# Performance work log

Hardware: AMD Instinct MI355X
Metric: run time of the kernel (lower is better)

The kernel has to match this reference:

```python
import jax, jax.numpy as jnp
import numpy as np
from functools import partial

# --- constants from module init / yolov5 NMS conventions ---
CONF_THRES = 0.25
IOU_THRES = 0.45
PATCH_CONF = 0.001
GN = jnp.array([640.0, 640.0, 640.0, 640.0])  # img_size[[1,0,1,0]]
MAX_WH = 4096.0       # per-class NMS offset trick
K_CLEAN = 256         # fixed-size cap for clean detections (max_det=1000 effectively)
K_PATCH = 1024        # fixed-size cap for patch detections (max_det=30000 effectively)
MAXDET_CLEAN = 1000
MAXDET_PATCH = 30000
B, N, NC = 8, 25200, 80


def xywh2xyxy(x):
    xy, wh = x[..., :2], x[..., 2:4]
    return jnp.concatenate([xy - wh * 0.5, xy + wh * 0.5], axis=-1)


def pairwise_iou(a, b):
    # a: [A,4], b: [B,4] -> [A,B] jaccard overlap (same math as IoU.get_iou)
    tl = jnp.maximum(a[:, None, :2], b[None, :, :2])
    br = jnp.minimum(a[:, None, 2:], b[None, :, 2:])
    wh = jnp.clip(br - tl, 0.0)
    inter = wh[..., 0] * wh[..., 1]
    area_a = (a[:, 2] - a[:, 0]) * (a[:, 3] - a[:, 1])
    area_b = (b[:, 2] - b[:, 0]) * (b[:, 3] - b[:, 1])
    return inter / (area_a[:, None] + area_b[None, :] - inter)


def greedy_nms(iou_mat, valid, iou_thres):
    # iou_mat: [K,K] (score-sorted order), valid: [K] bool. Greedy suppression.
    K = valid.shape[0]
    j = jnp.arange(K)

    def body(i, keep):
        suppress = keep[i] & (iou_mat[i] > iou_thres) & (j > i)
        return keep & ~suppress

    return jax.lax.fori_loop(0, K, body, valid)


def _nms_single(pred, conf_thres, K, max_det):
    # pred: [N, 5+nc] raw yolov5 prediction for one image
    boxes = xywh2xyxy(pred[:, :4])
    obj = pred[:, 4]
    cls_scores = pred[:, 5:] * obj[:, None]          # conf = obj * cls
    conf = cls_scores.max(axis=-1)
    cls = jnp.argmax(cls_scores, axis=-1).astype(pred.dtype)
    valid = (obj > conf_thres) & (conf > conf_thres)
    mscore = jnp.where(valid, conf, -1.0)
    _, idx = jax.lax.top_k(mscore, K)                # fixed-size candidate prefilter
    bk, ck, vk = boxes[idx], cls[idx], valid[idx]
    off_boxes = bk + (ck * MAX_WH)[:, None]          # class-offset NMS
    iou = pairwise_iou(off_boxes, off_boxes)
    keep = greedy_nms(jax.lax.stop_gradient(iou), vk, IOU_THRES)
    keep = keep & (jnp.cumsum(keep.astype(jnp.int32)) <= max_det)
    return bk, ck, keep


def _forward(output_clean, output_patch):
    nms_clean = jax.vmap(lambda p: _nms_single(p, CONF_THRES, K_CLEAN, MAXDET_CLEAN))
    nms_patch = jax.vmap(lambda p: _nms_single(p, PATCH_CONF, K_PATCH, MAXDET_PATCH))
    bc, cc, kc = nms_clean(output_clean)   # [B,Kc,4],[B,Kc],[B,Kc]
    bp, cp, kp = nms_patch(output_patch)   # [B,Kp,4],[B,Kp],[B,Kp]
    bc_n = bc / GN
    bp_n = bp / GN

    def per_img(bp_i, cp_i, kp_i, bc_i, cc_i, kc_i):
        iou = pairwise_iou(bp_i, bc_i)                       # [Kp, Kc]
        match = kp_i[:, None] & (cp_i[:, None] == cc_i[None, :])
        tm = jnp.max(jnp.where(match, iou, 0.0), axis=0)     # max IoU per clean det
        return jnp.sum(jnp.where(kc_i, tm, 0.0)), jnp.sum(kc_i.astype(jnp.float32))

    sums, counts = jax.vmap(per_img)(bp_n, cp, kp, bc_n, cc, kc)
    total, cnt = sums.sum(), counts.sum()
    return jnp.where(cnt > 0, 1.0 - total / jnp.maximum(cnt, 1.0), 1.0)


def setup_inputs() -> dict:
    key = jax.random.key(0)
    k1, k2 = jax.random.split(key)

    def make(k):
        kxy, kwh, ko, kc = jax.random.split(k, 4)
        xy = jax.random.uniform(kxy, (B, N, 2)) * 608.0 + 16.0   # centers in-frame
        wh = jax.random.uniform(kwh, (B, N, 2)) * 96.0 + 8.0     # plausible box sizes
        obj = jax.random.uniform(ko, (B, N, 1))
        cls = jax.random.uniform(kc, (B, N, NC))
        return jnp.concatenate([xy, wh, obj, cls], axis=-1)

    return {"output_clean": make(k1), "output_patch": make(k2)}


def reference(output_clean, output_patch):
    return _forward(output_clean, output_patch)
```

## Files before the change

### kernel.cpp

```cpp
#include <hip/hip_runtime.h>

#define N_ANCH 25200
#define NCLS   80
#define ROW    85
#define NIMG   16
#define KMAX   1024
#define NBINS  1024
#define CAND_CAP 4096
#define SC2_RPC 16
#define SC2_CPI 1575
#define SC2_CFLOATS (SC2_RPC*ROW)
#define SC2_BPI 96
#define SC2_WPI 192
#define PCHUNK 64
#define CCNT_STRIDE 16

typedef unsigned long long u64;
typedef unsigned int u32;

#define OFF_KEYS 0ull
#define OFF_HIST 3225600ull
#define OFF_TBIN 3291136ull
#define OFF_CCNT 3291200ull
#define OFF_CAND 3292224ull
#define OFF_SEL  3816512ull
#define OFF_BOX  3947584ull
#define OFF_CLS  4209728ull
#define OFF_RINIT 4275264ull
#define OFF_KEEP 4277312ull
#define WS_NEED  4342848ull
#define ZERO_BYTES 66624ull

#define DMA16(gsrc, ldst) \
    __builtin_amdgcn_global_load_lds( \
        (const __attribute__((address_space(1))) void*)(gsrc), \
        (__attribute__((address_space(3))) void*)(ldst), 16, 0, 0)

__device__ __forceinline__ int key_bin(u64 key) {
    u32 hi = (u32)(key >> 32);
    if (hi == 0u) return 0;
    float conf = __uint_as_float(hi - 0x40000000u);
    int b = 1 + (int)(conf * 1022.0f);
    return b > 1023 ? 1023 : b;
}

__device__ __forceinline__ u64 readlane64(u64 v, int src) {
    u32 lo = (u32)__builtin_amdgcn_readlane((int)(u32)(v & 0xffffffffull), src);
    u32 hi = (u32)__builtin_amdgcn_readlane((int)(u32)(v >> 32), src);
    return ((u64)hi << 32) | (u64)lo;
}

__device__ __forceinline__ u64 shfl64_xor(u64 v, int m) {
    int lo = __shfl_xor((int)(u32)(v & 0xffffffffull), m, 64);
    int hi = __shfl_xor((int)(u32)(v >> 32), m, 64);
    return ((u64)(u32)hi << 32) | (u64)(u32)lo;
}

__device__ __forceinline__ void sc_issue(const float* __restrict__ img, int ch,
                                         int lane, float* buf)
{
    const float* s = img + (size_t)ch * SC2_CFLOATS;
    #pragma unroll
    for (int u = 0; u < 5; ++u)
        DMA16(s + u * 256 + lane * 4, buf + u * 256);
    if (lane < 20)
        DMA16(s + 1280 + lane * 4, buf + 1280);
}

__device__ __forceinline__ void sc_compute(int b, int c, int lane, const float* buf,
                                           u64* __restrict__ keys, int* bh)
{
    const int r = lane & 15, h = lane >> 4;
    const float* p = buf + r * ROW;
    const float obj = p[4];
    float best = -1.0f; int bc = 0;
    #pragma unroll
    for (int d = 0; d < 20; ++d) {
        const float s = p[5 + h * 20 + d] * obj;
        if (s > best) { best = s; bc = h * 20 + d; }
    }
    #pragma unroll
    for (int m = 16; m <= 32; m <<= 1) {
        const float o = __shfl_xor(best, m, 64);
        const int  oc = __shfl_xor(bc, m, 64);
        if (o > best || (o == best && oc < bc)) { best = o; bc = oc; }
    }
    if (h == 0) {
        const int n = c * SC2_RPC + r;
        const float th = (b < 8) ? 0.25f : 0.001f;
        const bool valid = (obj > th) && (best > th);
        const u32 hi = valid ? (__float_as_uint(best) + 0x40000000u) : 0u;
        if (valid) {
            int bin = 1 + (int)(best * 1022.0f);
            if (bin > 1023) bin = 1023;
            atomicAdd(&bh[bin], 1);
        }
        const u32 nbar = 32767u - (u32)n;
        keys[(size_t)b * N_ANCH + n] =
            ((u64)hi << 32) | ((u64)nbar << 8) | (u64)(u32)bc;
    }
}

__global__ __launch_bounds__(128) void k_score(const float* __restrict__ clean,
                                               const float* __restrict__ patch,
                                               u64* __restrict__ keys,
                                               int* __restrict__ hist)
{
    __shared__ float lds[2][2][SC2_CFLOATS];
    __shared__ int bh[NBINS];
    const int t = threadIdx.x;
    const int wv = t >> 6, lane = t & 63;
    const int b = blockIdx.x / SC2_BPI;
    const int blk = blockIdx.x - b * SC2_BPI;
    const int wimg = blk * 2 + wv;
    for (int i = t; i < NBINS; i += 128) bh[i] = 0;
    __syncthreads();
    const float* img = (b < 8) ? clean + (size_t)b * N_ANCH * ROW
                               : patch + (size_t)(b - 8) * N_ANCH * ROW;
    int cur = 0;
    sc_issue(img, wimg, lane, &lds[wv][0][0]);
    for (int c = wimg; c < SC2_CPI; c += SC2_WPI) {
        const int cn = c + SC2_WPI;
        if (cn < SC2_CPI) {
            sc_issue(img, cn, lane, &lds[wv][cur ^ 1][0]);
            asm volatile("s_waitcnt vmcnt(6)" ::: "memory");
        } else {
            asm volatile("s_waitcnt vmcnt(0)" ::: "memory");
        }
        __builtin_amdgcn_sched_barrier(0);
        sc_compute(b, c, lane, &lds[wv][cur][0], keys, bh);
        cur ^= 1;
    }
    __syncthreads();
    for (int i = t; i < NBINS; i += 128)
        if (bh[i]) atomicAdd(&hist[b * NBINS + i], bh[i]);
}

__global__ __launch_bounds__(256) void k_thresh(const int* __restrict__ hist,
                                                int* __restrict__ tbin)
{
    __shared__ int arr[256];
    const int b = blockIdx.x;
    const int t = threadIdx.x;
    int hh[4];
    hh[0] = hist[b * NBINS + 4 * t + 0];
    hh[1] = hist[b * NBINS + 4 * t + 1];
    hh[2] = hist[b * NBINS + 4 * t + 2];
    hh[3] = hist[b * NBINS + 4 * t + 3];
    const int r = hh[0] + hh[1] + hh[2] + hh[3];
    arr[t] = r;
    __syncthreads();
    for (int off = 1; off < 256; off <<= 1) {
        int v = (t + off < 256) ? arr[t + off] : 0;
        __syncthreads();
        arr[t] += v;
        __syncthreads();
    }
    const int K = (b < 8) ? 256 : 1024;
    int cb = arr[t] - r;
    for (int d = 3; d >= 0; --d) {
        int ca = cb + hh[d];
        if (cb < K && ca >= K) tbin[b] = 4 * t + d;
        cb = ca;
    }
}

__global__ __launch_bounds__(256) void k_compact(const u64* __restrict__ keys,
                                                 const int* __restrict__ tbin,
                                                 int* __restrict__ ccnt,
                                                 u64* __restrict__ cand)
{
    const int b = blockIdx.x;
    const int T = tbin[b];
    const u64* kp = keys + (size_t)b * N_ANCH;
    const int start = blockIdx.y * 1575;
    const int lane = threadIdx.x & 63;
    #pragma unroll
    for (int it = 0; it < 7; ++it) {
        const int off = it * 256 + threadIdx.x;
        const bool in = off < 1575;
        const u64 key = in ? kp[start + off] : 0ull;
        const bool cnd = in && (key_bin(key) >= T);
        const u64 bal = __ballot(cnd);
        if (bal) {
            int base = 0;
            if (lane == 0) base = atomicAdd(&ccnt[b * CCNT_STRIDE], __popcll(bal));
            base = __shfl(base, 0, 64);
            if (cnd) {
                const int pos = base + __popcll(bal & ((1ull << lane) - 1ull));
                if (pos < CAND_CAP) cand[(size_t)b * CAND_CAP + pos] = key;
            }
        }
    }
}

__global__ __launch_bounds__(1024) void k_sort(const u64* __restrict__ cand,
                                               const int* __restrict__ ccnt,
                                               u64* __restrict__ sel)
{
    __shared__ u64 sk[CAND_CAP];
    const int b = blockIdx.x;
    const int C = min(ccnt[b * CCNT_STRIDE], CAND_CAP);
    const int t = threadIdx.x;
    u64 e0, e1, e2, e3;
    e0 = (t < C) ? cand[(size_t)b * CAND_CAP + t] : 0ull;
    e1 = (1024 + t < C) ? cand[(size_t)b * CAND_CAP + 1024 + t] : 0ull;
    e2 = (2048 + t < C) ? cand[(size_t)b * CAND_CAP + 2048 + t] : 0ull;
    e3 = (3072 + t < C) ? cand[(size_t)b * CAND_CAP + 3072 + t] : 0ull;
    #define CSWAP_D(a, c) { if ((a) < (c)) { u64 _t = (a); (a) = (c); (c) = _t; } }
    #define CSWAP_A(a, c) { if ((a) > (c)) { u64 _t = (a); (a) = (c); (c) = _t; } }
    for (int k = 2; k <= 4096; k <<= 1) {
        for (int j = k >> 1; j > 0; j >>= 1) {
            if (j >= 1024) {
                if (j == 2048) { CSWAP_D(e0, e2); CSWAP_D(e1, e3); }
                else {
                    if (k == 4096) { CSWAP_D(e0, e1); CSWAP_D(e2, e3); }
                    else           { CSWAP_D(e0, e1); CSWAP_A(e2, e3); }
                }
            } else if (j >= 64) {
                __syncthreads();
                sk[t] = e0; sk[1024 + t] = e1; sk[2048 + t] = e2; sk[3072 + t] = e3;
                __syncthreads();
                const int tp = t ^ j;
                #pragma unroll
                for (int p = 0; p < 4; ++p) {
                    const int i = p * 1024 + t;
                    const u64 cv = (p == 0) ? e0 : (p == 1) ? e1 : (p == 2) ? e2 : e3;
                    const u64 o = sk[p * 1024 + tp];
                    const bool take_max = (((i & k) == 0) == ((t & j) == 0));
                    const u64 mx = cv > o ? cv : o;
                    const u64 mn = cv > o ? o : cv;
                    const u64 nv = take_max ? mx : mn;
                    if (p == 0) e0 = nv; else if (p == 1) e1 = nv;
                    else if (p == 2) e2 = nv; else e3 = nv;
                }
            } else {
                #pragma unroll
                for (int p = 0; p < 4; ++p) {
                    const int i = p * 1024 + t;
                    const u64 cv = (p == 0) ? e0 : (p == 1) ? e1 : (p == 2) ? e2 : e3;
                    const u64 o = shfl64_xor(cv, j);
                    const bool take_max = (((i & k) == 0) == ((t & j) == 0));
                    const u64 mx = cv > o ? cv : o;
                    const u64 mn = cv > o ? o : cv;
                    const u64 nv = take_max ? mx : mn;
                    if (p == 0) e0 = nv; else if (p == 1) e1 = nv;
                    else if (p == 2) e2 = nv; else e3 = nv;
                }
            }
        }
    }
    const int K = (b < 8) ? 256 : 1024;
    if (t < K) sel[b * KMAX + t] = e0;
    #undef CSWAP_D
    #undef CSWAP_A
}

__global__ __launch_bounds__(1024) void k_nms_mask(const float* __restrict__ clean,
                                                   const float* __restrict__ patch,
                                                   const u64* __restrict__ sel,
                                                   float4* __restrict__ boxes,
                                                   int* __restrict__ cls,
                                                   u64* __restrict__ rinit,
                                                   u64* __restrict__ mask,
                                                   u64* __restrict__ diag)
{
    __shared__ float4 bx[KMAX];
    __shared__ float ar[KMAX];
    const int b = blockIdx.x, y = blockIdx.y;
    const int K = (b < 8) ? 256 : 1024;
    const int row0 = y * 64;
    if (row0 >= K) return;
    const int t = threadIdx.x;
    {
        const u64 key = (t < K) ? sel[b * KMAX + t] : 0ull;
        const u32 hi = (u32)(key >> 32);
        const bool valid = (t < K) && (hi != 0u);
        const u64 bal = __ballot(valid);
        if (y == 0 && (t & 63) == 0) rinit[b * 16 + (t >> 6)] = ~bal;
        if (t < K) {
            const int n = 32767 - (int)((key >> 8) & 0x7FFFu);
            const int c = (int)(key & 0x7Fu);
            const float* src = ((b < 8) ? (clean + (size_t)b * N_ANCH * ROW)
                                        : (patch + (size_t)(b - 8) * N_ANCH * ROW))
                               + (size_t)n * ROW;
            const float x = src[0], yy = src[1], w = src[2], h = src[3];
            const float4 raw = make_float4(x - w * 0.5f, yy - h * 0.5f,
                                           x + w * 0.5f, yy + h * 0.5f);
            if (y == 0) { boxes[b * KMAX + t] = raw; cls[b * KMAX + t] = c; }
            const float off = (float)c * 4096.0f;
            const float4 ob = make_float4(raw.x + off, raw.y + off,
                                          raw.z + off, raw.w + off);
            bx[t] = ob;
            ar[t] = (ob.z - ob.x) * (ob.w - ob.y);
        }
    }
    __syncthreads();
    const int w   = t >> 6;
    const int row = row0 + (t & 63);
    u64* dst = mask + ((size_t)b * KMAX + row) * 16 + w;
    if (((w << 6) + 63) <= row0 && row0 > 0) { *dst = 0ull; return; }
    const float4 bi = bx[row];
    const float ai = ar[row];
    const int jbase = w << 6;
    u64 m = 0;
    #pragma unroll 8
    for (int k = 0; k < 64; ++k) {
        const int j = jbase + k;
        const float4 bj = bx[j];
        const float ax = fmaxf(bi.x, bj.x), ay = fmaxf(bi.y, bj.y);
        const float bx2 = fminf(bi.z, bj.z), by2 = fminf(bi.w, bj.w);
        const float iw = fmaxf(bx2 - ax, 0.f), ih = fmaxf(by2 - ay, 0.f);
        const float inter = iw * ih;
        const float iou = inter / (ai + ar[j] - inter);
        if (j > row && iou > 0.45f) m |= (1ull << k);
    }
    *dst = m;
    if (w == (row0 >> 6)) diag[(size_t)b * KMAX + row] = m;
}

__global__ __launch_bounds__(1024) void k_nms_scan(const u64* __restrict__ mask,
                                                   const u64* __restrict__ diag,
                                                   const u64* __restrict__ rinit,
                                                   int* __restrict__ keep)
{
    extern __shared__ u64 smem[];
    const int b = blockIdx.x;
    const int K = (b < 8) ? 256 : 1024;
    const int W = K >> 6;
    const int t = threadIdx.x;
    u64* smask = smem;
    u64* sdiag = smem + (size_t)K * 16;
    {
        const float4* s4 = (const float4*)(mask + (size_t)b * KMAX * 16);
        float4* d4 = (float4*)smask;
        const int n4 = (K * 16) >> 1;
        for (int i = t; i < n4; i += 1024) d4[i] = s4[i];
        const float4* s4d = (const float4*)(diag + (size_t)b * KMAX);
        float4* d4d = (float4*)sdiag;
        for (int i = t; i < (K >> 1); i += 1024) d4d[i] = s4d[i];
    }
    __syncthreads();
    if (t >= 64) return;
    const int lane = t;
    const int q = lane >> 4;
    const int wl = lane & 15;
    u64 w_remv = rinit[b * 16 + wl];
    u64 ow = readlane64(w_remv, 0);
    u64 dj = sdiag[lane];
    for (int g = 0; g < W; ++g) {
        u64 nz = __ballot(dj != 0ull);
        u64 o = ow;
        while (nz) {
            const int j = (int)__builtin_ctzll(nz);
            nz &= nz - 1;
            if (!((o >> j) & 1ull)) o |= readlane64(dj, j);
        }
        const u64 kept = ~o;
        if (g + 1 < W) dj = sdiag[(g + 1) * 64 + lane];
        const u64* mrow = smask + (size_t)(g * 64 + q * 16) * 16 + wl;
        const u32 kg = (u32)((kept >> (q * 16)) & 0xFFFFull);
        u64 a0 = 0, a1 = 0;
        #pragma unroll
        for (int i = 0; i < 16; i += 2) {
            const u64 m0 = mrow[(size_t)(i + 0) * 16];
            const u64 m1 = mrow[(size_t)(i + 1) * 16];
            a0 |= ((kg >> i) & 1u) ? m0 : 0ull;
            a1 |= ((kg >> (i + 1)) & 1u) ? m1 : 0ull;
        }
        u64 part = a0 | a1;
        part |= shfl64_xor(part, 16);
        part |= shfl64_xor(part, 32);
        w_remv |= part;
        if (g + 1 < W) ow = readlane64(w_remv, g + 1);
    }
    if (lane < W) {
        #pragma unroll
        for (int k = 0; k < 64; ++k)
            keep[b * KMAX + lane * 64 + k] = (int)(((w_remv >> k) & 1) ^ 1ull);
    }
}

__global__ __launch_bounds__(256) void k_match_partial(const float4* __restrict__ boxes,
                                                       const int* __restrict__ cls,
                                                       const int* __restrict__ keep,
                                                       float* __restrict__ pmax)
{
    __shared__ float4 pb[PCHUNK];
    __shared__ float par[PCHUNK];
    __shared__ int pcls[PCHUNK];
    const int c = blockIdx.x;
    const int p = blockIdx.y;
    const int bp = 8 + c;
    const int t = threadIdx.x;
    if (t < PCHUNK) {
        const int i = p * PCHUNK + t;
        const float4 v = boxes[bp * KMAX + i];
        pb[t] = v;
        par[t] = (v.z - v.x) * (v.w - v.y);
        pcls[t] = keep[bp * KMAX + i] ? cls[bp * KMAX + i] : -1;
    }
    __syncthreads();
    const float4 bc = boxes[c * KMAX + t];
    const int cc = cls[c * KMAX + t];
    const float area_c = (bc.z - bc.x) * (bc.w - bc.y);
    float tm = 0.f;
    #pragma unroll 8
    for (int i = 0; i < PCHUNK; ++i) {
        const float4 bi = pb[i];
        const float ax = fmaxf(bi.x, bc.x), ay = fmaxf(bi.y, bc.y);
        const float bx2 = fminf(bi.z, bc.z), by2 = fminf(bi.w, bc.w);
        const float iw = fmaxf(bx2 - ax, 0.f), ih = fmaxf(by2 - ay, 0.f);
        const float inter = iw * ih;
        const float iou = inter / (par[i] + area_c - inter);
        tm = fmaxf(tm, (pcls[i] == cc) ? iou : 0.f);
    }
    pmax[(c * 16 + p) * 256 + t] = tm;
}

__global__ __launch_bounds__(256) void k_match_final(const float* __restrict__ pmax,
                                                     const int* __restrict__ keep,
                                                     float* __restrict__ out)
{
    __shared__ float red[8];
    const int t = threadIdx.x;
    float tot = 0.f, cn = 0.f;
    for (int c = 0; c < 8; ++c) {
        float tm = 0.f;
        #pragma unroll
        for (int p = 0; p < 16; ++p)
            tm = fmaxf(tm, pmax[(c * 16 + p) * 256 + t]);
        const int kc = keep[c * KMAX + t];
        float val = kc ? tm : 0.f;
        float cv  = kc ? 1.f : 0.f;
        for (int off = 32; off > 0; off >>= 1) {
            val += __shfl_down(val, off);
            cv  += __shfl_down(cv, off);
        }
        const int wv = t >> 6, lane = t & 63;
        if (lane == 0) { red[wv] = val; red[4 + wv] = cv; }
        __syncthreads();
        if (t == 0) {
            tot += red[0] + red[1] + red[2] + red[3];
            cn  += red[4] + red[5] + red[6] + red[7];
        }
        __syncthreads();
    }
    if (t == 0)
        out[0] = (cn > 0.f) ? (1.0f - tot / fmaxf(cn, 1.0f)) : 1.0f;
}

extern "C" void kernel_launch(void* const* d_in, const int* in_sizes, int n_in,
                              void* d_out, int out_size, void* d_ws, size_t ws_size,
                              hipStream_t stream)
{
    if (ws_size < WS_NEED) return;
    const float* clean = (const float*)d_in[0];
    const float* patch = (const float*)d_in[1];
    float* out = (float*)d_out;
    char* ws = (char*)d_ws;

    u64*    keys = (u64*)(ws + OFF_KEYS);
    u64*    mask = (u64*)(ws + OFF_KEYS);
    int*    hist = (int*)(ws + OFF_HIST);
    int*    tbin = (int*)(ws + OFF_TBIN);
    int*    ccnt = (int*)(ws + OFF_CCNT);
    u64*    cand = (u64*)(ws + OFF_CAND);
    u64*    diag = (u64*)(ws + OFF_CAND);
    float*  pmax = (float*)(ws + OFF_CAND);
    u64*    sel  = (u64*)(ws + OFF_SEL);
    float4* boxes = (float4*)(ws + OFF_BOX);
    int*    cls  = (int*)(ws + OFF_CLS);
    u64*    rinit = (u64*)(ws + OFF_RINIT);
    int*    keep = (int*)(ws + OFF_KEEP);

    hipMemsetAsync(ws + OFF_HIST, 0, ZERO_BYTES, stream);

    k_score<<<NIMG * SC2_BPI, 128, 0, stream>>>(clean, patch, keys, hist);
    k_thresh<<<NIMG, 256, 0, stream>>>(hist, tbin);
    k_compact<<<dim3(NIMG, 16), 256, 0, stream>>>(keys, tbin, ccnt, cand);
    k_sort<<<NIMG, 1024, 0, stream>>>(cand, ccnt, sel);
    k_nms_mask<<<dim3(NIMG, 16), 1024, 0, stream>>>(clean, patch, sel, boxes, cls,
                                                    rinit, mask, diag);
    k_nms_scan<<<NIMG, 1024, KMAX * 16 * 8 + KMAX * 8, stream>>>(mask, diag, rinit, keep);
    k_match_partial<<<dim3(8, 16), 256, 0, stream>>>(boxes, cls, keep, pmax);
    k_match_final<<<1, 256, 0, stream>>>(pmax, keep, out);
}
```

Baseline: 133.6 us.

## Fuse threshold, compaction and sort into one kernel; register-staged score loads

Merges the histogram-threshold, candidate compaction and bitonic sort kernels into a single per-image kernel. Candidates now go straight into shared memory, which removes two launches and the global candidate round trip. The scoring kernel swaps its async global-to-LDS DMA double buffering for register double buffering followed by an LDS store, and raises the block count per image. The trade-off is that compaction now runs on only 16 blocks, one per image, scanning 25200 keys each, so that phase has far less parallelism.

Measured after the change: 174.4 us. +30.5%, slower.

```diff
diff --git a/kernel.cpp b/kernel.cpp
--- a/kernel.cpp
+++ b/kernel.cpp
@@ -10,31 +10,23 @@
 #define SC2_RPC 16
 #define SC2_CPI 1575
 #define SC2_CFLOATS (SC2_RPC*ROW)
-#define SC2_BPI 96
-#define SC2_WPI 192
+#define SC3_BPI 160
+#define SC3_WPI 320
 #define PCHUNK 64
-#define CCNT_STRIDE 16
 
 typedef unsigned long long u64;
 typedef unsigned int u32;
 
 #define OFF_KEYS 0ull
 #define OFF_HIST 3225600ull
-#define OFF_TBIN 3291136ull
-#define OFF_CCNT 3291200ull
-#define OFF_CAND 3292224ull
-#define OFF_SEL  3816512ull
-#define OFF_BOX  3947584ull
-#define OFF_CLS  4209728ull
-#define OFF_RINIT 4275264ull
-#define OFF_KEEP 4277312ull
-#define WS_NEED  4342848ull
-#define ZERO_BYTES 66624ull
-
-#define DMA16(gsrc, ldst) \
-    __builtin_amdgcn_global_load_lds( \
-        (const __attribute__((address_space(1))) void*)(gsrc), \
-        (__attribute__((address_space(3))) void*)(ldst), 16, 0, 0)
+#define OFF_DIAG 3291136ull
+#define OFF_SEL  3422208ull
+#define OFF_BOX  3553280ull
+#define OFF_CLS  3815424ull
+#define OFF_RINIT 3880960ull
+#define OFF_KEEP 3883008ull
+#define WS_NEED  3948544ull
+#define ZERO_BYTES 65536ull
 
 __device__ __forceinline__ int key_bin(u64 key) {
     u32 hi = (u32)(key >> 32);
@@ -56,15 +48,27 @@
     return ((u64)(u32)hi << 32) | (u64)(u32)lo;
 }
 
-__device__ __forceinline__ void sc_issue(const float* __restrict__ img, int ch,
-                                         int lane, float* buf)
-{
-    const float* s = img + (size_t)ch * SC2_CFLOATS;
-    #pragma unroll
-    for (int u = 0; u < 5; ++u)
-        DMA16(s + u * 256 + lane * 4, buf + u * 256);
-    if (lane < 20)
-        DMA16(s + 1280 + lane * 4, buf + 1280);
+__device__ __forceinline__ void ld6(const float* __restrict__ img, int ch, int lane,
+                                    float4* f)
+{
+    const float4* s = (const float4*)(img + (size_t)ch * SC2_CFLOATS);
+    f[0] = s[lane];
+    f[1] = s[lane + 64];
+    f[2] = s[lane + 128];
+    f[3] = s[lane + 192];
+    f[4] = s[lane + 256];
+    if (lane < 20) f[5] = s[lane + 320];
+}
+
+__device__ __forceinline__ void st6(float* buf, int lane, const float4* f)
+{
+    float4* d = (float4*)buf;
+    d[lane]       = f[0];
+    d[lane + 64]  = f[1];
+    d[lane + 128] = f[2];
+    d[lane + 192] = f[3];
+    d[lane + 256] = f[4];
+    if (lane < 20) d[lane + 320] = f[5];
 }
 
 __device__ __forceinline__ void sc_compute(int b, int c, int lane, const float* buf,
@@ -106,107 +110,89 @@
                                                u64* __restrict__ keys,
                                                int* __restrict__ hist)
 {
-    __shared__ float lds[2][2][SC2_CFLOATS];
+    __shared__ float lds[2][SC2_CFLOATS];
     __shared__ int bh[NBINS];
     const int t = threadIdx.x;
     const int wv = t >> 6, lane = t & 63;
-    const int b = blockIdx.x / SC2_BPI;
-    const int blk = blockIdx.x - b * SC2_BPI;
+    const int b = blockIdx.x / SC3_BPI;
+    const int blk = blockIdx.x - b * SC3_BPI;
     const int wimg = blk * 2 + wv;
     for (int i = t; i < NBINS; i += 128) bh[i] = 0;
     __syncthreads();
     const float* img = (b < 8) ? clean + (size_t)b * N_ANCH * ROW
                                : patch + (size_t)(b - 8) * N_ANCH * ROW;
-    int cur = 0;
-    sc_issue(img, wimg, lane, &lds[wv][0][0]);
-    for (int c = wimg; c < SC2_CPI; c += SC2_WPI) {
-        const int cn = c + SC2_WPI;
-        if (cn < SC2_CPI) {
-            sc_issue(img, cn, lane, &lds[wv][cur ^ 1][0]);
-            asm volatile("s_waitcnt vmcnt(6)" ::: "memory");
+    float* buf = &lds[wv][0];
+    float4 fA[6], fB[6];
+    bool useA = true;
+    if (wimg < SC2_CPI) ld6(img, wimg, lane, fA);
+    for (int c = wimg; c < SC2_CPI; c += SC3_WPI) {
+        const int cn = c + SC3_WPI;
+        if (useA) {
+            if (cn < SC2_CPI) ld6(img, cn, lane, fB);
+            st6(buf, lane, fA);
         } else {
-            asm volatile("s_waitcnt vmcnt(0)" ::: "memory");
-        }
-        __builtin_amdgcn_sched_barrier(0);
-        sc_compute(b, c, lane, &lds[wv][cur][0], keys, bh);
-        cur ^= 1;
+            if (cn < SC2_CPI) ld6(img, cn, lane, fA);
+            st6(buf, lane, fB);
+        }
+        sc_compute(b, c, lane, buf, keys, bh);
+        useA = !useA;
     }
     __syncthreads();
     for (int i = t; i < NBINS; i += 128)
         if (bh[i]) atomicAdd(&hist[b * NBINS + i], bh[i]);
 }
 
-__global__ __launch_bounds__(256) void k_thresh(const int* __restrict__ hist,
-                                                int* __restrict__ tbin)
-{
-    __shared__ int arr[256];
+__global__ __launch_bounds__(1024) void k_tcs(const u64* __restrict__ keys,
+                                              const int* __restrict__ hist,
+                                              u64* __restrict__ sel)
+{
+    __shared__ u64 sk[CAND_CAP];
+    __shared__ int arr[NBINS];
+    __shared__ int cnt;
+    __shared__ int Tsh;
     const int b = blockIdx.x;
     const int t = threadIdx.x;
-    int hh[4];
-    hh[0] = hist[b * NBINS + 4 * t + 0];
-    hh[1] = hist[b * NBINS + 4 * t + 1];
-    hh[2] = hist[b * NBINS + 4 * t + 2];
-    hh[3] = hist[b * NBINS + 4 * t + 3];
-    const int r = hh[0] + hh[1] + hh[2] + hh[3];
-    arr[t] = r;
-    __syncthreads();
-    for (int off = 1; off < 256; off <<= 1) {
-        int v = (t + off < 256) ? arr[t + off] : 0;
+    const int K = (b < 8) ? 256 : 1024;
+    if (t == 0) { cnt = 0; Tsh = 0; }
+    const int h = hist[b * NBINS + t];
+    arr[t] = h;
+    __syncthreads();
+    for (int off = 1; off < NBINS; off <<= 1) {
+        int v = (t + off < NBINS) ? arr[t + off] : 0;
         __syncthreads();
         arr[t] += v;
         __syncthreads();
     }
-    const int K = (b < 8) ? 256 : 1024;
-    int cb = arr[t] - r;
-    for (int d = 3; d >= 0; --d) {
-        int ca = cb + hh[d];
-        if (cb < K && ca >= K) tbin[b] = 4 * t + d;
-        cb = ca;
-    }
-}
-
-__global__ __launch_bounds__(256) void k_compact(const u64* __restrict__ keys,
-                                                 const int* __restrict__ tbin,
-                                                 int* __restrict__ ccnt,
-                                                 u64* __restrict__ cand)
-{
-    const int b = blockIdx.x;
-    const int T = tbin[b];
+    if ((arr[t] - h) < K && arr[t] >= K) Tsh = t;
+    __syncthreads();
+    const int T = Tsh;
     const u64* kp = keys + (size_t)b * N_ANCH;
-    const int start = blockIdx.y * 1575;
-    const int lane = threadIdx.x & 63;
+    const int lane = t & 63;
     #pragma unroll
-    for (int it = 0; it < 7; ++it) {
-        const int off = it * 256 + threadIdx.x;
-        const bool in = off < 1575;
-        const u64 key = in ? kp[start + off] : 0ull;
+    for (int it = 0; it < 25; ++it) {
+        const int i = it * 1024 + t;
+        const bool in = i < N_ANCH;
+        const u64 key = in ? kp[i] : 0ull;
         const bool cnd = in && (key_bin(key) >= T);
         const u64 bal = __ballot(cnd);
         if (bal) {
             int base = 0;
-            if (lane == 0) base = atomicAdd(&ccnt[b * CCNT_STRIDE], __popcll(bal));
+            if (lane == 0) base = atomicAdd(&cnt, __popcll(bal));
             base = __shfl(base, 0, 64);
             if (cnd) {
                 const int pos = base + __popcll(bal & ((1ull << lane) - 1ull));
-                if (pos < CAND_CAP) cand[(size_t)b * CAND_CAP + pos] = key;
+                if (pos < CAND_CAP) sk[pos] = key;
             }
         }
     }
-}
-
-__global__ __launch_bounds__(1024) void k_sort(const u64* __restrict__ cand,
-                                               const int* __restrict__ ccnt,
-                                               u64* __restrict__ sel)
-{
-    __shared__ u64 sk[CAND_CAP];
-    const int b = blockIdx.x;
-    const int C = min(ccnt[b * CCNT_STRIDE], CAND_CAP);
-    const int t = threadIdx.x;
+    __syncthreads();
+    const int C = min(cnt, CAND_CAP);
     u64 e0, e1, e2, e3;
-    e0 = (t < C) ? cand[(size_t)b * CAND_CAP + t] : 0ull;
-    e1 = (1024 + t < C) ? cand[(size_t)b * CAND_CAP + 1024 + t] : 0ull;
-    e2 = (2048 + t < C) ? cand[(size_t)b * CAND_CAP + 2048 + t] : 0ull;
-    e3 = (3072 + t < C) ? cand[(size_t)b * CAND_CAP + 3072 + t] : 0ull;
+    e0 = (t < C) ? sk[t] : 0ull;
+    e1 = (1024 + t < C) ? sk[1024 + t] : 0ull;
+    e2 = (2048 + t < C) ? sk[2048 + t] : 0ull;
+    e3 = (3072 + t < C) ? sk[3072 + t] : 0ull;
+    __syncthreads();
     #define CSWAP_D(a, c) { if ((a) < (c)) { u64 _t = (a); (a) = (c); (c) = _t; } }
     #define CSWAP_A(a, c) { if ((a) > (c)) { u64 _t = (a); (a) = (c); (c) = _t; } }
     for (int k = 2; k <= 4096; k <<= 1) {
@@ -250,7 +236,6 @@
             }
         }
     }
-    const int K = (b < 8) ? 256 : 1024;
     if (t < K) sel[b * KMAX + t] = e0;
     #undef CSWAP_D
     #undef CSWAP_A
@@ -463,11 +448,8 @@
     u64*    keys = (u64*)(ws + OFF_KEYS);
     u64*    mask = (u64*)(ws + OFF_KEYS);
     int*    hist = (int*)(ws + OFF_HIST);
-    int*    tbin = (int*)(ws + OFF_TBIN);
-    int*    ccnt = (int*)(ws + OFF_CCNT);
-    u64*    cand = (u64*)(ws + OFF_CAND);
-    u64*    diag = (u64*)(ws + OFF_CAND);
-    float*  pmax = (float*)(ws + OFF_CAND);
+    u64*    diag = (u64*)(ws + OFF_DIAG);
+    float*  pmax = (float*)(ws + OFF_DIAG);
     u64*    sel  = (u64*)(ws + OFF_SEL);
     float4* boxes = (float4*)(ws + OFF_BOX);
     int*    cls  = (int*)(ws + OFF_CLS);
@@ -476,10 +458,8 @@
 
     hipMemsetAsync(ws + OFF_HIST, 0, ZERO_BYTES, stream);
 
-    k_score<<<NIMG * SC2_BPI, 128, 0, stream>>>(clean, patch, keys, hist);
-    k_thresh<<<NIMG, 256, 0, stream>>>(hist, tbin);
-    k_compact<<<dim3(NIMG, 16), 256, 0, stream>>>(keys, tbin, ccnt, cand);
-    k_sort<<<NIMG, 1024, 0, stream>>>(cand, ccnt, sel);
+    k_score<<<NIMG * SC3_BPI, 128, 0, stream>>>(clean, patch, keys, hist);
+    k_tcs<<<NIMG, 1024, 0, stream>>>(keys, hist, sel);
     k_nms_mask<<<dim3(NIMG, 16), 1024, 0, stream>>>(clean, patch, sel, boxes, cls,
                                                     rinit, mask, diag);
     k_nms_scan<<<NIMG, 1024, KMAX * 16 * 8 + KMAX * 8, stream>>>(mask, diag, rinit, keep);
```
